# Optimization experiments

Hardware: AMD Instinct MI355X
Metric: run time of the kernel (lower is better)

## Reference

```python
import jax, jax.numpy as jnp
import numpy as np

D_MODEL = 96
D_STATE = 6
D_CONV = 9
D_INNER = 2 * D_MODEL          # expand = 2
DT_RANK = (D_MODEL + 15) // 16  # ceil(d_model/16) = 6
DIM_IN = 64
DIM_OUT = 64
BATCH = 16
SEQLEN = 4096


def setup_inputs() -> dict:
    key = jax.random.key(0)
    ks = jax.random.split(key, 12)
    def s(k, shape, scale=0.02):
        return jax.random.normal(k, shape, jnp.float32) * scale
    return {
        "x": jax.random.normal(ks[0], (BATCH, SEQLEN, D_MODEL), jnp.float32),
        # Mamba block params
        "in_proj_w": s(ks[1], (2 * D_INNER, D_MODEL)),
        "conv_w": s(ks[2], (D_INNER, D_CONV), 0.1),   # depthwise conv kernel
        "conv_b": jnp.zeros((D_INNER,), jnp.float32),
        "x_proj_w": s(ks[3], (DT_RANK + 2 * D_STATE, D_INNER)),
        "dt_proj_w": s(ks[4], (D_INNER, DT_RANK), 0.1),
        "dt_proj_b": s(ks[5], (D_INNER,), 0.1),
        "A_log": jnp.log(jnp.tile(jnp.arange(1, D_STATE + 1, dtype=jnp.float32), (D_INNER, 1))),
        "D_param": jnp.ones((D_INNER,), jnp.float32),
        "out_proj_w": s(ks[6], (D_MODEL, D_INNER)),
        "norm_w": jnp.ones((D_MODEL,), jnp.float32),  # RMSNorm weight
        # heads
        "out_fc_w": s(ks[7], (DIM_IN, D_MODEL)),
        "out_fc_b": jnp.zeros((DIM_IN,), jnp.float32),
        "mu_w": s(ks[8], (DIM_OUT, DIM_IN)),
        "mu_b": jnp.zeros((DIM_OUT,), jnp.float32),
        "sigma_w": s(ks[9], (DIM_OUT, DIM_IN)),
        "sigma_b": jnp.zeros((DIM_OUT,), jnp.float32),
    }


def _mamba_block(x, in_proj_w, conv_w, conv_b, x_proj_w, dt_proj_w, dt_proj_b,
                 A_log, D_param, out_proj_w):
    Bsz = x.shape[0]
    xz = jnp.einsum('bld,ed->ble', x, in_proj_w)          # (B,L,2*ED)
    xs, z = jnp.split(xz, 2, axis=-1)
    # causal depthwise conv1d (torch pads d_conv-1 both sides then trims right)
    xt = xs.transpose(0, 2, 1)                            # (B,ED,L)
    kern = conv_w[:, None, :]                             # (ED,1,K)
    xc = jax.lax.conv_general_dilated(xt, kern, window_strides=(1,),
                                      padding=[(D_CONV - 1, 0)],
                                      feature_group_count=D_INNER)
    xc = (xc + conv_b[None, :, None]).transpose(0, 2, 1)  # (B,L,ED)
    xc = jax.nn.silu(xc)
    dbc = jnp.einsum('ble,fe->blf', xc, x_proj_w)         # (B,L,dt_rank+2N)
    delta_r = dbc[..., :DT_RANK]
    Bm = dbc[..., DT_RANK:DT_RANK + D_STATE]              # (B,L,N)
    Cm = dbc[..., DT_RANK + D_STATE:]                     # (B,L,N)
    delta = jax.nn.softplus(jnp.einsum('blr,er->ble', delta_r, dt_proj_w) + dt_proj_b)
    A = -jnp.exp(A_log)                                   # (ED,N)
    deltaA = jnp.exp(delta[..., None] * A)                # (B,L,ED,N)
    BX = (delta * xc)[..., None] * Bm[:, :, None, :]      # (B,L,ED,N)

    def step(h, inputs):
        dA, bx = inputs
        h = dA * h + bx
        return h, h

    h0 = jnp.zeros((Bsz, D_INNER, D_STATE), x.dtype)
    _, hs = jax.lax.scan(step, h0, (deltaA.swapaxes(0, 1), BX.swapaxes(0, 1)))
    y = jnp.einsum('lben,bln->ble', hs, Cm)               # (B,L,ED)
    y = y + D_param * xc
    y = y * jax.nn.silu(z)
    return jnp.einsum('ble,de->bld', y, out_proj_w)       # (B,L,D)


def reference(x, in_proj_w, conv_w, conv_b, x_proj_w, dt_proj_w, dt_proj_b,
              A_log, D_param, out_proj_w, norm_w,
              out_fc_w, out_fc_b, mu_w, mu_b, sigma_w, sigma_b):
    # residual block: x + mixer(RMSNorm(x))   (dropout is identity at eval)
    h = x * jax.lax.rsqrt(jnp.mean(x * x, axis=-1, keepdims=True) + 1e-5) * norm_w
    out = x + _mamba_block(h, in_proj_w, conv_w, conv_b, x_proj_w,
                           dt_proj_w, dt_proj_b, A_log, D_param, out_proj_w)
    e = out.mean(axis=1)                                  # (B,D)
    feat = jax.nn.elu(jnp.tanh(e @ out_fc_w.T + out_fc_b))
    mu = feat @ mu_w.T + mu_b
    sigma = jax.nn.elu(feat @ sigma_w.T + sigma_b) + 1.0 + 1e-14
    return (feat, mu, sigma)
```

## Files before the change

### kernel.cpp

```cpp
#include <hip/hip_runtime.h>
#include <math.h>

#define BATCH 16
#define SEQLEN 4096
#define D_MODEL 96
#define D_STATE 6
#define D_CONV 9
#define D_INNER 192
#define DT_RANK 6
#define NPOS (BATCH * SEQLEN)

#define NC2 128
#define CT2 (SEQLEN / NC2)
#define NSEG 16
#define CPS (NC2 / NSEG)

#define OFF_XS    0L
#define OFF_Z     (OFF_XS   + (long)NPOS * 96)
#define OFF_OUT4  (OFF_Z    + (long)NPOS * 96)
#define OFF_SEG   (OFF_OUT4 + (long)BATCH * NC2 * 5 * 192 * 4)
#define OFF_XPART (OFF_SEG  + (long)BATCH * NSEG * 5 * 192 * 4)
#define OFF_XPB   (OFF_XPART + (long)(NPOS / 64) * 96)

typedef short v8s __attribute__((ext_vector_type(8)));
typedef float v4f __attribute__((ext_vector_type(4)));

__device__ __forceinline__ float silu_fast(float v) {
    return __fdividef(v, 1.0f + __expf(-v));
}
__device__ __forceinline__ float softplus_fast(float v) {
    return (v > 20.0f) ? v : __logf(1.0f + __expf(v));
}
__device__ __forceinline__ float eluf(float v) {
    return (v > 0.0f) ? v : expm1f(v);
}
__device__ __forceinline__ unsigned int pack_bf16(float a, float b) {
    unsigned int ua = __float_as_uint(a), ub = __float_as_uint(b);
    ua += 0x7FFFu + ((ua >> 16) & 1u);
    ub += 0x7FFFu + ((ub >> 16) & 1u);
    return (ua >> 16) | (ub & 0xFFFF0000u);
}
__device__ __forceinline__ unsigned short bf16h(float v) {
    unsigned int u = __float_as_uint(v);
    u += 0x7FFFu + ((u >> 16) & 1u);
    return (unsigned short)(u >> 16);
}
__device__ __forceinline__ float bf2f(unsigned short h) {
    return __uint_as_float(((unsigned int)h) << 16);
}

#define TP1 64
__global__ __launch_bounds__(256, 2) void k1_rmsnorm_inproj(
    const float* __restrict__ x, const float* __restrict__ W,
    const float* __restrict__ norm_w, const float* __restrict__ x_proj_w,
    unsigned short* __restrict__ xs, unsigned short* __restrict__ z,
    float* __restrict__ xpart, unsigned int* __restrict__ xpb)
{
    __shared__ unsigned int s_ovl[7680];
    __shared__ unsigned int s_hA[64 * 52];
    __shared__ float s_part[TP1][4];
    __shared__ float s_scale[TP1];
    float* hRow = (float*)s_ovl;
    unsigned int* WB = s_ovl;

    const int tid = threadIdx.x;
    const long p0 = (long)blockIdx.x * TP1;

    {
        const float4* x4 = (const float4*)&x[p0 * 96];
        for (int i = tid; i < TP1 * 24; i += 256) {
            int p = i / 24, dq = i - p * 24;
            float4 v = x4[i];
            float* hr = &hRow[p * 101 + dq * 4];
            hr[0] = v.x; hr[1] = v.y; hr[2] = v.z; hr[3] = v.w;
        }
    }
    __syncthreads();

    {
        int p = tid >> 2, g = tid & 3;
        float ss = 0.0f;
        for (int d = g; d < 96; d += 4) { float v = hRow[p * 101 + d]; ss += v * v; }
        s_part[p][g] = ss;
    }
    __syncthreads();

    if (tid < TP1) {
        float ss = s_part[tid][0] + s_part[tid][1] + s_part[tid][2] + s_part[tid][3];
        s_scale[tid] = 1.0f / sqrtf(ss / 96.0f + 1e-5f);
    } else if (tid < TP1 + 96) {
        int d = tid - TP1;
        float s = 0.0f;
        for (int p = 0; p < TP1; p++) s += hRow[p * 101 + d];
        xpart[(long)blockIdx.x * 96 + d] = s;
    }
    __syncthreads();

    {
        const float2* nw2 = (const float2*)norm_w;
        for (int i = tid; i < TP1 * 48; i += 256) {
            int p = i / 48, dp = i - p * 48;
            float sc = s_scale[p];
            float2 nv = nw2[dp];
            float v0 = hRow[p * 101 + 2 * dp]     * sc * nv.x;
            float v1 = hRow[p * 101 + 2 * dp + 1] * sc * nv.y;
            s_hA[p * 52 + dp] = pack_bf16(v0, v1);
        }
    }
    __syncthreads();

    const int wave = tid >> 6, lane = tid & 63;
    const int quad = lane >> 4, ln = lane & 15;
    const int n0 = wave * 96;
    unsigned int* WBw = WB + wave * 1920;

    v4f acc[4][6];
#pragma unroll
    for (int mt = 0; mt < 4; mt++)
#pragma unroll
        for (int nt = 0; nt < 6; nt++) acc[mt][nt] = (v4f){0.f, 0.f, 0.f, 0.f};

    for (int kc = 0; kc < 3; kc++) {
#pragma unroll 8
        for (int ii = 0; ii < 24; ii++) {
            int i = lane + ii * 64;
            int jp = i >> 4, kp = i & 15;
            const float2 wv = *(const float2*)&W[(n0 + jp) * 96 + kc * 32 + 2 * kp];
            WBw[jp * 20 + kp] = pack_bf16(wv.x, wv.y);
        }
        v8s bfh[4];
#pragma unroll
        for (int mt = 0; mt < 4; mt++)
            bfh[mt] = *(const v8s*)&s_hA[(mt * 16 + ln) * 52 + kc * 16 + quad * 4];
#pragma unroll
        for (int nt = 0; nt < 6; nt++) {
            v8s aw = *(const v8s*)&WBw[(nt * 16 + ln) * 20 + quad * 4];
#pragma unroll
            for (int mt = 0; mt < 4; mt++)
                acc[mt][nt] = __builtin_amdgcn_mfma_f32_16x16x32_bf16(
                    aw, bfh[mt], acc[mt][nt], 0, 0, 0);
        }
    }

    unsigned short* dst = (wave < 2) ? xs : z;
    const bool is_z = (wave >= 2);
    const int jb = (wave & 1) * 96;
#pragma unroll
    for (int mt = 0; mt < 4; mt++) {
        long pos = p0 + mt * 16 + ln;
#pragma unroll
        for (int nt = 0; nt < 6; nt++) {
            float f0 = acc[mt][nt][0], f1 = acc[mt][nt][1];
            float f2 = acc[mt][nt][2], f3 = acc[mt][nt][3];
            if (is_z) {
                f0 = silu_fast(f0); f1 = silu_fast(f1);
                f2 = silu_fast(f2); f3 = silu_fast(f3);
            }
            uint2 v;
            v.x = pack_bf16(f0, f1);
            v.y = pack_bf16(f2, f3);
            *(uint2*)&dst[pos * D_INNER + jb + nt * 16 + quad * 4] = v;
        }
    }

    if (blockIdx.x == 0) {
        for (int i = tid; i < 18 * 96; i += 256) {
            const float2 wv = *(const float2*)&x_proj_w[2 * i];
            xpb[i] = pack_bf16(wv.x, wv.y);
        }
    }
}

#define SXSTR 200
__global__ __launch_bounds__(192, 4) void k2f_conv_scan(
    const unsigned short* __restrict__ xs, const unsigned short* __restrict__ z,
    const float* __restrict__ conv_w, const float* __restrict__ conv_b,
    const unsigned short* __restrict__ xpb,
    const float* __restrict__ dt_w, const float* __restrict__ dt_b,
    const float* __restrict__ A_log, const float* __restrict__ D_param,
    float4* __restrict__ out4)
{
    __shared__ unsigned short sxc[CT2 * SXSTR];
    __shared__ float sMeta[CT2][20];
    const int e = threadIdx.x;
    const int c = blockIdx.x & (NC2 - 1);
    const int b = blockIdx.x >> 7;
    const int l0 = c * CT2;
    const long brow = (long)b * SEQLEN;

    float cw[D_CONV];
#pragma unroll
    for (int k = 0; k < D_CONV; k++) cw[k] = conv_w[e * D_CONV + k];
    const float cb = conv_b[e];
    float win[D_CONV];
#pragma unroll
    for (int k = 0; k < 8; k++) {
        int ll = l0 - 8 + k;
        win[k] = (ll >= 0) ? bf2f(xs[(brow + ll) * D_INNER + e]) : 0.0f;
    }
#pragma unroll
    for (int r = 0; r < CT2; r++) {
        win[8] = bf2f(xs[(brow + l0 + r) * D_INNER + e]);
        float s = cb;
#pragma unroll
        for (int k = 0; k < D_CONV; k++) s += win[k] * cw[k];
        sxc[r * SXSTR + e] = bf16h(silu_fast(s));
#pragma unroll
        for (int k = 0; k < 8; k++) win[k] = win[k + 1];
    }

    const unsigned short* zp = &z[(brow + l0) * D_INNER + e];
    float zv[CT2];
#pragma unroll
    for (int t = 0; t < CT2; t++) zv[t] = bf2f(zp[(long)t * D_INNER]);
    __syncthreads();

    {
        const int wave = e >> 6, lane = e & 63;
        const int quad = lane >> 4, ln = lane & 15;
        if (wave < 2) {
            const int mt = wave;
            const int r1 = (ln < 2) ? 16 + ln : 0;
            v4f dacc[2];
            dacc[0] = (v4f){0.f, 0.f, 0.f, 0.f};
            dacc[1] = (v4f){0.f, 0.f, 0.f, 0.f};
#pragma unroll
            for (int kc = 0; kc < 6; kc++) {
                v8s af  = *(const v8s*)&sxc[(mt * 16 + ln) * SXSTR + kc * 32 + quad * 8];
                v8s bf0 = *(const v8s*)&xpb[ln * 192 + kc * 32 + quad * 8];
                v8s bf1 = *(const v8s*)&xpb[r1 * 192 + kc * 32 + quad * 8];
                dacc[0] = __builtin_amdgcn_mfma_f32_16x16x32_bf16(af, bf0, dacc[0], 0, 0, 0);
                dacc[1] = __builtin_amdgcn_mfma_f32_16x16x32_bf16(af, bf1, dacc[1], 0, 0, 0);
            }
#pragma unroll
            for (int nt = 0; nt < 2; nt++) {
                int f = nt * 16 + ln;
                if (f < 18) {
                    int col = (f < 6) ? f : f + 2;
#pragma unroll
                    for (int r = 0; r < 4; r++)
                        sMeta[mt * 16 + quad * 4 + r][col] = dacc[nt][r];
                }
            }
        }
    }
    __syncthreads();

    float a[D_STATE];
#pragma unroll
    for (int n = 0; n < D_STATE; n++) a[n] = -__expf(A_log[e * D_STATE + n]);
    float dtw[DT_RANK];
#pragma unroll
    for (int q = 0; q < DT_RANK; q++) dtw[q] = dt_w[e * DT_RANK + q];
    const float dtb = dt_b[e];
    const float Dv = D_param[e];
    const float a0 = a[0];

    bool pok = true;
#pragma unroll
    for (int n = 1; n < D_STATE; n++)
        pok = pok && (fabsf(a[n] - (float)(n + 1) * a0)
                      <= 1e-4f * (float)(n + 1) * fabsf(a0));
    unsigned long long pmask = __ballot(pok);

    float S[D_STATE], G[D_STATE];
#pragma unroll
    for (int n = 0; n < D_STATE; n++) { S[n] = 0.0f; G[n] = 0.0f; }
    float ysum0 = 0.0f;

    if (pmask == 0xFFFFFFFFFFFFFFFFull) {
        float Pa = 1.0f;
#pragma unroll 2
        for (int t = 0; t < CT2; t++) {
            const float4* m4 = (const float4*)&sMeta[t][0];
            float4 m0 = m4[0], m1 = m4[1], mB0 = m4[2], mB1 = m4[3], mC = m4[4];
            float Bv[6] = {mB0.x, mB0.y, mB0.z, mB0.w, mB1.x, mB1.y};
            float Cv[6] = {mB1.z, mB1.w, mC.x, mC.y, mC.z, mC.w};
            float dr = dtb + m0.x * dtw[0] + m0.y * dtw[1] + m0.z * dtw[2]
                     + m0.w * dtw[3] + m1.x * dtw[4] + m1.y * dtw[5];
            float dl = softplus_fast(dr);
            float xv = bf2f(sxc[t * SXSTR + e]);
            float zw = zv[t];
            float dx = dl * xv;
            float y = Dv * xv;
            float E = __expf(dl * a0);
            Pa *= E;
            float dA = E;
            float w = zw * Pa;
#pragma unroll
            for (int n = 0; n < D_STATE; n++) {
                S[n] = dA * S[n] + dx * Bv[n];
                y += S[n] * Cv[n];
                G[n] += w * Cv[n];
                dA *= E;
                w *= Pa;
            }
            ysum0 += zw * y;
        }
        long ob = (long)(b * NC2 + c) * 5 * 192 + e;
        float P1 = Pa, P2 = P1 * Pa, P3 = P2 * Pa, P4 = P3 * Pa, P5 = P4 * Pa, P6 = P5 * Pa;
        float4 q0, q1, q2, q3, q4;
        q0.x=P1; q0.y=P2; q0.z=P3; q0.w=P4;
        q1.x=P5; q1.y=P6; q1.z=S[0]; q1.w=S[1];
        q2.x=S[2]; q2.y=S[3]; q2.z=S[4]; q2.w=S[5];
        q3.x=G[0]; q3.y=G[1]; q3.z=G[2]; q3.w=G[3];
        q4.x=G[4]; q4.y=G[5]; q4.z=ysum0; q4.w=0.0f;
        out4[ob          ] = q0;
        out4[ob + 192    ] = q1;
        out4[ob + 2 * 192] = q2;
        out4[ob + 3 * 192] = q3;
        out4[ob + 4 * 192] = q4;
    } else {
        float P[D_STATE];
#pragma unroll
        for (int n = 0; n < D_STATE; n++) P[n] = 1.0f;
#pragma unroll 2
        for (int t = 0; t < CT2; t++) {
            const float4* m4 = (const float4*)&sMeta[t][0];
            float4 m0 = m4[0], m1 = m4[1], mB0 = m4[2], mB1 = m4[3], mC = m4[4];
            float Bv[6] = {mB0.x, mB0.y, mB0.z, mB0.w, mB1.x, mB1.y};
            float Cv[6] = {mB1.z, mB1.w, mC.x, mC.y, mC.z, mC.w};
            float dr = dtb + m0.x * dtw[0] + m0.y * dtw[1] + m0.z * dtw[2]
                     + m0.w * dtw[3] + m1.x * dtw[4] + m1.y * dtw[5];
            float dl = softplus_fast(dr);
            float xv = bf2f(sxc[t * SXSTR + e]);
            float zw = zv[t];
            float dx = dl * xv;
            float y = Dv * xv;
#pragma unroll
            for (int n = 0; n < D_STATE; n++) {
                float dA = __expf(dl * a[n]);
                S[n] = dA * S[n] + dx * Bv[n];
                P[n] *= dA;
                y += S[n] * Cv[n];
                G[n] += zw * P[n] * Cv[n];
            }
            ysum0 += zw * y;
        }
        long ob = (long)(b * NC2 + c) * 5 * 192 + e;
        float4 q0, q1, q2, q3, q4;
        q0.x=P[0]; q0.y=P[1]; q0.z=P[2]; q0.w=P[3];
        q1.x=P[4]; q1.y=P[5]; q1.z=S[0]; q1.w=S[1];
        q2.x=S[2]; q2.y=S[3]; q2.z=S[4]; q2.w=S[5];
        q3.x=G[0]; q3.y=G[1]; q3.z=G[2]; q3.w=G[3];
        q4.x=G[4]; q4.y=G[5]; q4.z=ysum0; q4.w=0.0f;
        out4[ob          ] = q0;
        out4[ob + 192    ] = q1;
        out4[ob + 2 * 192] = q2;
        out4[ob + 3 * 192] = q3;
        out4[ob + 4 * 192] = q4;
    }
}

__global__ __launch_bounds__(192) void k4_seg(
    const float4* __restrict__ out4, float4* __restrict__ seg4)
{
    const int e = threadIdx.x;
    const int s = blockIdx.x & (NSEG - 1);
    const int b = blockIdx.x >> 4;

    float H[D_STATE], Gq[D_STATE], Pp[D_STATE];
#pragma unroll
    for (int n = 0; n < D_STATE; n++) { H[n] = 0.0f; Gq[n] = 0.0f; Pp[n] = 1.0f; }
    float yb = 0.0f;
#pragma unroll 2
    for (int cc = 0; cc < CPS; cc++) {
        int c = s * CPS + cc;
        long ob = (long)(b * NC2 + c) * 5 * 192 + e;
        float4 q0 = out4[ob];
        float4 q1 = out4[ob + 192];
        float4 q2 = out4[ob + 2 * 192];
        float4 q3 = out4[ob + 3 * 192];
        float4 q4 = out4[ob + 4 * 192];
        float Pv[6] = {q0.x, q0.y, q0.z, q0.w, q1.x, q1.y};
        float Sv[6] = {q1.z, q1.w, q2.x, q2.y, q2.z, q2.w};
        float Gv[6] = {q3.x, q3.y, q3.z, q3.w, q4.x, q4.y};
        float g = 0.0f;
#pragma unroll
        for (int n = 0; n < D_STATE; n++) g += Gv[n] * H[n];
        yb += q4.z + g;
#pragma unroll
        for (int n = 0; n < D_STATE; n++) {
            Gq[n] += Gv[n] * Pp[n];
            H[n] = Pv[n] * H[n] + Sv[n];
            Pp[n] *= Pv[n];
        }
    }
    long sb = (long)(b * NSEG + s) * 5 * 192 + e;
    float4 q0, q1, q2, q3, q4;
    q0.x=Pp[0]; q0.y=Pp[1]; q0.z=Pp[2]; q0.w=Pp[3];
    q1.x=Pp[4]; q1.y=Pp[5]; q1.z=H[0]; q1.w=H[1];
    q2.x=H[2]; q2.y=H[3]; q2.z=H[4]; q2.w=H[5];
    q3.x=Gq[0]; q3.y=Gq[1]; q3.z=Gq[2]; q3.w=Gq[3];
    q4.x=Gq[4]; q4.y=Gq[5]; q4.z=yb; q4.w=0.0f;
    seg4[sb          ] = q0;
    seg4[sb + 192    ] = q1;
    seg4[sb + 2 * 192] = q2;
    seg4[sb + 3 * 192] = q3;
    seg4[sb + 4 * 192] = q4;
}

__global__ __launch_bounds__(192) void k4_head(
    const float4* __restrict__ seg4, const float* __restrict__ xpart,
    const float* __restrict__ Wout,
    const float* __restrict__ fc_w, const float* __restrict__ fc_b,
    const float* __restrict__ mu_w, const float* __restrict__ mu_b,
    const float* __restrict__ sg_w, const float* __restrict__ sg_b,
    float* __restrict__ out)
{
    __shared__ float ybar[D_INNER];
    __shared__ float sxb[D_MODEL];
    __shared__ float evec[D_MODEL];
    __shared__ float feat_s[64];
    const int e = threadIdx.x;
    const int b = blockIdx.x;

    float H[D_STATE];
#pragma unroll
    for (int n = 0; n < D_STATE; n++) H[n] = 0.0f;
    float yb = 0.0f;
#pragma unroll 4
    for (int s = 0; s < NSEG; s++) {
        long ob = (long)(b * NSEG + s) * 5 * 192 + e;
        float4 q0 = seg4[ob];
        float4 q1 = seg4[ob + 192];
        float4 q2 = seg4[ob + 2 * 192];
        float4 q3 = seg4[ob + 3 * 192];
        float4 q4 = seg4[ob + 4 * 192];
        float Pv[6] = {q0.x, q0.y, q0.z, q0.w, q1.x, q1.y};
        float Sv[6] = {q1.z, q1.w, q2.x, q2.y, q2.z, q2.w};
        float Gv[6] = {q3.x, q3.y, q3.z, q3.w, q4.x, q4.y};
        float g = 0.0f;
#pragma unroll
        for (int n = 0; n < D_STATE; n++) g += Gv[n] * H[n];
        yb += q4.z + g;
#pragma unroll
        for (int n = 0; n < D_STATE; n++) H[n] = Pv[n] * H[n] + Sv[n];
    }
    ybar[e] = yb;

    if (e < D_MODEL) {
        const float* xp = &xpart[(long)b * 64 * 96 + e];
        float s = 0.0f;
        for (int t = 0; t < 64; t++) s += xp[t * 96];
        sxb[e] = s;
    }
    __syncthreads();

    if (e < D_MODEL) {
        float s = sxb[e];
        const float* wrow = &Wout[e * D_INNER];
        for (int e2 = 0; e2 < D_INNER; e2++) s += ybar[e2] * wrow[e2];
        evec[e] = s / (float)SEQLEN;
    }
    __syncthreads();

    if (e < 64) {
        float s = fc_b[e];
        const float* wrow = &fc_w[e * D_MODEL];
        for (int d = 0; d < D_MODEL; d++) s += evec[d] * wrow[d];
        float f = eluf(tanhf(s));
        feat_s[e] = f;
        out[b * 64 + e] = f;
    }
    __syncthreads();

    if (e < 64) {
        float smu = mu_b[e], ssg = sg_b[e];
        const float* mrow = &mu_w[e * 64];
        const float* srow = &sg_w[e * 64];
        for (int i = 0; i < 64; i++) {
            smu += feat_s[i] * mrow[i];
            ssg += feat_s[i] * srow[i];
        }
        out[1024 + b * 64 + e] = smu;
        out[2048 + b * 64 + e] = eluf(ssg) + 1.0f + 1e-14f;
    }
}

extern "C" void kernel_launch(void* const* d_in, const int* in_sizes, int n_in,
                              void* d_out, int out_size, void* d_ws, size_t ws_size,
                              hipStream_t stream) {
    const float* x         = (const float*)d_in[0];
    const float* in_proj_w = (const float*)d_in[1];
    const float* conv_w    = (const float*)d_in[2];
    const float* conv_b    = (const float*)d_in[3];
    const float* x_proj_w  = (const float*)d_in[4];
    const float* dt_proj_w = (const float*)d_in[5];
    const float* dt_proj_b = (const float*)d_in[6];
    const float* A_log     = (const float*)d_in[7];
    const float* D_param   = (const float*)d_in[8];
    const float* out_proj_w= (const float*)d_in[9];
    const float* norm_w    = (const float*)d_in[10];
    const float* out_fc_w  = (const float*)d_in[11];
    const float* out_fc_b  = (const float*)d_in[12];
    const float* mu_w      = (const float*)d_in[13];
    const float* mu_b      = (const float*)d_in[14];
    const float* sigma_w   = (const float*)d_in[15];
    const float* sigma_b   = (const float*)d_in[16];
    float* ws = (float*)d_ws;
    float* out = (float*)d_out;

    k1_rmsnorm_inproj<<<NPOS / TP1, 256, 0, stream>>>(
        x, in_proj_w, norm_w, x_proj_w,
        (unsigned short*)(ws + OFF_XS), (unsigned short*)(ws + OFF_Z),
        ws + OFF_XPART, (unsigned int*)(ws + OFF_XPB));

    k2f_conv_scan<<<BATCH * NC2, 192, 0, stream>>>(
        (const unsigned short*)(ws + OFF_XS), (const unsigned short*)(ws + OFF_Z),
        conv_w, conv_b, (const unsigned short*)(ws + OFF_XPB),
        dt_proj_w, dt_proj_b, A_log, D_param,
        (float4*)(ws + OFF_OUT4));

    k4_seg<<<BATCH * NSEG, 192, 0, stream>>>(
        (const float4*)(ws + OFF_OUT4), (float4*)(ws + OFF_SEG));

    k4_head<<<BATCH, 192, 0, stream>>>(
        (const float4*)(ws + OFF_SEG), ws + OFF_XPART, out_proj_w,
        out_fc_w, out_fc_b, mu_w, mu_b, sigma_w, sigma_b, out);
}
```

Baseline: 195.6 us.

## Pre-pack in_proj weights to bf16 once and read them from global in k1

Adds a small k0_pack kernel that converts in_proj_w and x_proj_w to bf16 once per call, replacing the per-block fp32 load, convert and LDS staging of the weight tile inside k1. The k1 MFMA loop now loads weight fragments straight from the packed global buffer, relying on L2 and cache reuse. The tile shrinks to 32 positions and occupancy rises to 4 blocks per CU, which doubles the xpart partial sums that the head kernel reduces. The cost is an extra kernel launch and more global weight traffic per block in exchange for dropping the LDS staging and redundant conversion.

```diff
diff --git a/kernel.cpp b/kernel.cpp
--- a/kernel.cpp
+++ b/kernel.cpp
@@ -20,7 +20,8 @@
 #define OFF_OUT4  (OFF_Z    + (long)NPOS * 96)
 #define OFF_SEG   (OFF_OUT4 + (long)BATCH * NC2 * 5 * 192 * 4)
 #define OFF_XPART (OFF_SEG  + (long)BATCH * NSEG * 5 * 192 * 4)
-#define OFF_XPB   (OFF_XPART + (long)(NPOS / 64) * 96)
+#define OFF_XPB   (OFF_XPART + (long)(NPOS / 32) * 96)
+#define OFF_WB16  (OFF_XPB  + 18 * 96)
 
 typedef short v8s __attribute__((ext_vector_type(8)));
 typedef float v4f __attribute__((ext_vector_type(4)));
@@ -49,19 +50,34 @@
     return __uint_as_float(((unsigned int)h) << 16);
 }
 
-#define TP1 64
-__global__ __launch_bounds__(256, 2) void k1_rmsnorm_inproj(
-    const float* __restrict__ x, const float* __restrict__ W,
-    const float* __restrict__ norm_w, const float* __restrict__ x_proj_w,
+#define K0_W (384 * 48)
+#define K0_X (18 * 96)
+__global__ __launch_bounds__(256) void k0_pack(
+    const float* __restrict__ W, const float* __restrict__ x_proj_w,
+    unsigned int* __restrict__ wb16, unsigned int* __restrict__ xpb)
+{
+    int i = blockIdx.x * 256 + threadIdx.x;
+    if (i < K0_W) {
+        const float2 wv = *(const float2*)&W[2 * i];
+        wb16[i] = pack_bf16(wv.x, wv.y);
+    } else if (i < K0_W + K0_X) {
+        int j = i - K0_W;
+        const float2 wv = *(const float2*)&x_proj_w[2 * j];
+        xpb[j] = pack_bf16(wv.x, wv.y);
+    }
+}
+
+#define TP1 32
+__global__ __launch_bounds__(256, 4) void k1_rmsnorm_inproj(
+    const float* __restrict__ x, const unsigned short* __restrict__ wb16,
+    const float* __restrict__ norm_w,
     unsigned short* __restrict__ xs, unsigned short* __restrict__ z,
-    float* __restrict__ xpart, unsigned int* __restrict__ xpb)
+    float* __restrict__ xpart)
 {
-    __shared__ unsigned int s_ovl[7680];
-    __shared__ unsigned int s_hA[64 * 52];
-    __shared__ float s_part[TP1][4];
+    __shared__ float hRow[TP1 * 100];
+    __shared__ unsigned int s_hA[TP1 * 52];
+    __shared__ float s_part[TP1][8];
     __shared__ float s_scale[TP1];
-    float* hRow = (float*)s_ovl;
-    unsigned int* WB = s_ovl;
 
     const int tid = threadIdx.x;
     const long p0 = (long)blockIdx.x * TP1;
@@ -70,28 +86,28 @@
         const float4* x4 = (const float4*)&x[p0 * 96];
         for (int i = tid; i < TP1 * 24; i += 256) {
             int p = i / 24, dq = i - p * 24;
-            float4 v = x4[i];
-            float* hr = &hRow[p * 101 + dq * 4];
-            hr[0] = v.x; hr[1] = v.y; hr[2] = v.z; hr[3] = v.w;
+            *(float4*)&hRow[p * 100 + dq * 4] = x4[i];
         }
     }
     __syncthreads();
 
     {
-        int p = tid >> 2, g = tid & 3;
+        int p = tid >> 3, g = tid & 7;
         float ss = 0.0f;
-        for (int d = g; d < 96; d += 4) { float v = hRow[p * 101 + d]; ss += v * v; }
+        for (int d = g; d < 96; d += 8) { float v = hRow[p * 100 + d]; ss += v * v; }
         s_part[p][g] = ss;
     }
     __syncthreads();
 
     if (tid < TP1) {
-        float ss = s_part[tid][0] + s_part[tid][1] + s_part[tid][2] + s_part[tid][3];
+        float ss = 0.0f;
+#pragma unroll
+        for (int g = 0; g < 8; g++) ss += s_part[tid][g];
         s_scale[tid] = 1.0f / sqrtf(ss / 96.0f + 1e-5f);
     } else if (tid < TP1 + 96) {
         int d = tid - TP1;
         float s = 0.0f;
-        for (int p = 0; p < TP1; p++) s += hRow[p * 101 + d];
+        for (int p = 0; p < TP1; p++) s += hRow[p * 100 + d];
         xpart[(long)blockIdx.x * 96 + d] = s;
     }
     __syncthreads();
@@ -102,8 +118,8 @@
             int p = i / 48, dp = i - p * 48;
             float sc = s_scale[p];
             float2 nv = nw2[dp];
-            float v0 = hRow[p * 101 + 2 * dp]     * sc * nv.x;
-            float v1 = hRow[p * 101 + 2 * dp + 1] * sc * nv.y;
+            float v0 = hRow[p * 100 + 2 * dp]     * sc * nv.x;
+            float v1 = hRow[p * 100 + 2 * dp + 1] * sc * nv.y;
             s_hA[p * 52 + dp] = pack_bf16(v0, v1);
         }
     }
@@ -112,33 +128,23 @@
     const int wave = tid >> 6, lane = tid & 63;
     const int quad = lane >> 4, ln = lane & 15;
     const int n0 = wave * 96;
-    unsigned int* WBw = WB + wave * 1920;
-
-    v4f acc[4][6];
-#pragma unroll
-    for (int mt = 0; mt < 4; mt++)
+
+    v4f acc[2][6];
+#pragma unroll
+    for (int mt = 0; mt < 2; mt++)
 #pragma unroll
         for (int nt = 0; nt < 6; nt++) acc[mt][nt] = (v4f){0.f, 0.f, 0.f, 0.f};
 
     for (int kc = 0; kc < 3; kc++) {
-#pragma unroll 8
-        for (int ii = 0; ii < 24; ii++) {
-            int i = lane + ii * 64;
-            int jp = i >> 4, kp = i & 15;
-            const float2 wv = *(const float2*)&W[(n0 + jp) * 96 + kc * 32 + 2 * kp];
-            WBw[jp * 20 + kp] = pack_bf16(wv.x, wv.y);
-        }
-        v8s bfh[4];
-#pragma unroll
-        for (int mt = 0; mt < 4; mt++)
+        v8s bfh[2];
+#pragma unroll
+        for (int mt = 0; mt < 2; mt++)
             bfh[mt] = *(const v8s*)&s_hA[(mt * 16 + ln) * 52 + kc * 16 + quad * 4];
 #pragma unroll
         for (int nt = 0; nt < 6; nt++) {
-            v8s aw = *(const v8s*)&WBw[(nt * 16 + ln) * 20 + quad * 4];
-#pragma unroll
-            for (int mt = 0; mt < 4; mt++)
-                acc[mt][nt] = __builtin_amdgcn_mfma_f32_16x16x32_bf16(
-                    aw, bfh[mt], acc[mt][nt], 0, 0, 0);
+            v8s aw = *(const v8s*)&wb16[(n0 + nt * 16 + ln) * 96 + kc * 32 + quad * 8];
+            acc[0][nt] = __builtin_amdgcn_mfma_f32_16x16x32_bf16(aw, bfh[0], acc[0][nt], 0, 0, 0);
+            acc[1][nt] = __builtin_amdgcn_mfma_f32_16x16x32_bf16(aw, bfh[1], acc[1][nt], 0, 0, 0);
         }
     }
 
@@ -146,7 +152,7 @@
     const bool is_z = (wave >= 2);
     const int jb = (wave & 1) * 96;
 #pragma unroll
-    for (int mt = 0; mt < 4; mt++) {
+    for (int mt = 0; mt < 2; mt++) {
         long pos = p0 + mt * 16 + ln;
 #pragma unroll
         for (int nt = 0; nt < 6; nt++) {
@@ -160,13 +166,6 @@
             v.x = pack_bf16(f0, f1);
             v.y = pack_bf16(f2, f3);
             *(uint2*)&dst[pos * D_INNER + jb + nt * 16 + quad * 4] = v;
-        }
-    }
-
-    if (blockIdx.x == 0) {
-        for (int i = tid; i < 18 * 96; i += 256) {
-            const float2 wv = *(const float2*)&x_proj_w[2 * i];
-            xpb[i] = pack_bf16(wv.x, wv.y);
         }
     }
 }
@@ -440,9 +439,9 @@
     ybar[e] = yb;
 
     if (e < D_MODEL) {
-        const float* xp = &xpart[(long)b * 64 * 96 + e];
+        const float* xp = &xpart[(long)b * 128 * 96 + e];
         float s = 0.0f;
-        for (int t = 0; t < 64; t++) s += xp[t * 96];
+        for (int t = 0; t < 128; t++) s += xp[t * 96];
         sxb[e] = s;
     }
     __syncthreads();
@@ -501,10 +500,14 @@
     float* ws = (float*)d_ws;
     float* out = (float*)d_out;
 
+    k0_pack<<<(K0_W + K0_X + 255) / 256, 256, 0, stream>>>(
+        in_proj_w, x_proj_w,
+        (unsigned int*)(ws + OFF_WB16), (unsigned int*)(ws + OFF_XPB));
+
     k1_rmsnorm_inproj<<<NPOS / TP1, 256, 0, stream>>>(
-        x, in_proj_w, norm_w, x_proj_w,
+        x, (const unsigned short*)(ws + OFF_WB16), norm_w,
         (unsigned short*)(ws + OFF_XS), (unsigned short*)(ws + OFF_Z),
-        ws + OFF_XPART, (unsigned int*)(ws + OFF_XPB));
+        ws + OFF_XPART);
 
     k2f_conv_scan<<<BATCH * NC2, 192, 0, stream>>>(
         (const unsigned short*)(ws + OFF_XS), (const unsigned short*)(ws + OFF_Z),
```

Result: no change. 195.1 us, median of 2 (-0.3%).
